# Kernel tuning notes

Measured on AMD Instinct MI355X. Metric: run time of the kernel, lower is better.

## Reference

```python
import jax, jax.numpy as jnp
import numpy as np

B, S, F, H = 4, 8192, 1024, 16
D = F // H  # k_dim = 64
EPS = 1e-6


def setup_inputs() -> dict:
    rng = jax.random.key(0)
    ks = jax.random.split(rng, 6)
    # xavier-normal-ish scale for square (F, F) kernels
    w_std = float(np.sqrt(2.0 / (F + F)))
    return {
        "query": jax.random.normal(ks[0], (B, S, F), jnp.float32),
        "key": jax.random.normal(ks[1], (B, S, F), jnp.float32),
        "value": jax.random.normal(ks[2], (B, S, F), jnp.float32),
        "Wq": jax.random.normal(ks[3], (F, F), jnp.float32) * w_std,
        "Wk": jax.random.normal(ks[4], (F, F), jnp.float32) * w_std,
        "Wv": jax.random.normal(ks[5], (F, F), jnp.float32) * w_std,
        # per-head LayerNorm params for K and V (galerkin branch): (H, D)
        "ln_k_scale": jnp.ones((H, D), jnp.float32),
        "ln_k_bias": jnp.zeros((H, D), jnp.float32),
        "ln_v_scale": jnp.ones((H, D), jnp.float32),
        "ln_v_bias": jnp.zeros((H, D), jnp.float32),
    }


def _per_head_layernorm(x, scale, bias):
    # x: (B, H, N, D); scale/bias: (H, D) -> broadcast per head
    mu = jnp.mean(x, axis=-1, keepdims=True)
    var = jnp.var(x, axis=-1, keepdims=True)
    xn = (x - mu) * jax.lax.rsqrt(var + EPS)
    return xn * scale[None, :, None, :] + bias[None, :, None, :]


def reference(query, key, value, Wq, Wk, Wv, ln_k_scale, ln_k_bias, ln_v_scale, ln_v_bias):
    # QKV projections (no bias), then the module's raw contiguous reshape
    # (B, S, F) -> (B, H, S, D)  [NOT a head transpose -- faithful to source]
    q = jnp.matmul(query, Wq).reshape(B, H, -1, D)
    k = jnp.matmul(key, Wk).reshape(B, H, -1, D)
    v = jnp.matmul(value, Wv).reshape(B, H, -1, D)
    # galerkin: per-head LayerNorm on K and V only
    k = _per_head_layernorm(k, ln_k_scale, ln_k_bias)
    v = _per_head_layernorm(v, ln_v_scale, ln_v_bias)
    # linear (galerkin) attention: p_attn = K^T V / seq_len; out = Q p_attn
    seq_len = v.shape[-2]
    p_attn = jnp.einsum('bhnd,bhne->bhde', k, v) / seq_len  # (B, H, D, D)
    x = jnp.einsum('bhnd,bhde->bhne', q, p_attn)            # (B, H, N, D)
    att_output = x.reshape(B, -1, H * D)                    # (B, S, F)
    return (att_output, p_attn)
```

## Files before the change

### kernel.cpp

```cpp
#include <hip/hip_runtime.h>
#include <hip/hip_bf16.h>
#include <stdint.h>

#define DEVI __device__ __forceinline__

typedef __attribute__((ext_vector_type(8))) short bf16x8;
typedef __attribute__((ext_vector_type(4))) float f32x4;

static constexpr int Bb = 4, Ss = 8192, Ff = 1024, Hh = 16, Dd = 64;
static constexpr int Mm = Bb * Ss;
static constexpr int Kk = Ff;
static constexpr int PROJ_ELEMS = Mm * Ff;

DEVI ushort f2bf(float f) {
  uint32_t u = __builtin_bit_cast(uint32_t, f);
  u += 0x7fffu + ((u >> 16) & 1u);
  return (ushort)(u >> 16);
}
DEVI float bf2f(ushort u) { return __builtin_bit_cast(float, (uint32_t)u << 16); }

DEVI uint32_t pack2(float a, float b) {
  return (uint32_t)f2bf(a) | ((uint32_t)f2bf(b) << 16);
}

DEVI void async16(void* lds, const void* g) {
  __builtin_amdgcn_global_load_lds((const __attribute__((address_space(1))) void*)g,
                                   (__attribute__((address_space(3))) void*)lds,
                                   16, 0, 0);
}

__global__ __launch_bounds__(256) void wt_kernel(const float* __restrict__ Wq,
                                                 const float* __restrict__ Wk,
                                                 const float* __restrict__ Wv,
                                                 ushort* __restrict__ wt) {
  __shared__ float tile[64][65];
  int b = blockIdx.x;
  const int w = b >> 8; b &= 255;
  const int kt = b >> 4, nt = b & 15;
  const float* Wsrc = (w == 0) ? Wq : ((w == 1) ? Wk : Wv);
  ushort* dst = wt + (size_t)w * 1024 * 1024;
  const int t = threadIdx.x;
  const int r = t >> 6, c = t & 63;
#pragma unroll
  for (int i = 0; i < 16; i++) {
    const int kk = kt * 64 + r + i * 4;
    tile[r + i * 4][c] = Wsrc[(size_t)kk * 1024 + nt * 64 + c];
  }
  __syncthreads();
#pragma unroll
  for (int i = 0; i < 16; i++) {
    const int nn = nt * 64 + r + i * 4;
    dst[(size_t)nn * 1024 + kt * 64 + c] = f2bf(tile[c][r + i * 4]);
  }
}

__global__ __launch_bounds__(256, 3) void gemm_qkv_kernel(
    const float* __restrict__ Aq, const float* __restrict__ Ak,
    const float* __restrict__ Av, const ushort* __restrict__ Wt,
    ushort* __restrict__ Cout,
    const float* __restrict__ ksc, const float* __restrict__ kbi,
    const float* __restrict__ vsc, const float* __restrict__ vbi) {
  __shared__ __align__(16) ushort As[128][64];
  __shared__ __align__(16) ushort Bs[128][64];

  const int bx0 = blockIdx.x;
  const int bx = (bx0 & 7) * 768 + (bx0 >> 3);
  const int proj = bx >> 11;
  const int t2 = bx & 2047;
  const int mt = t2 >> 3;
  const int nt = t2 & 7;
  const float* A = (proj == 0) ? Aq : ((proj == 1) ? Ak : Av);
  const ushort* Bw = Wt + (size_t)proj * 1024 * 1024;
  ushort* C = Cout + (size_t)proj * PROJ_ELEMS;
  const int m0 = mt * 128, n0 = nt * 128;
  const int tid = threadIdx.x;
  const int lane = tid & 63;
  const int wave = tid >> 6;
  const int wy = wave >> 1, wx = wave & 1;

  const int ar = tid >> 3;
  const int ac = (tid & 7) * 8;
  const float* Abase = A + (size_t)m0 * Kk;

  const f32x4 fzero = {0.0f, 0.0f, 0.0f, 0.0f};
  f32x4 acc[4][4];
#pragma unroll
  for (int i = 0; i < 4; i++)
#pragma unroll
    for (int j = 0; j < 4; j++) acc[i][j] = fzero;

  for (int k0 = 0; k0 < Kk; k0 += 64) {
#pragma unroll
    for (int j = 0; j < 4; j++) {
      const int seg = wave * 4 + j;
      const int brow = seg * 8 + (lane >> 3);
      const int bcol = (lane & 7) * 8;
      async16(&Bs[seg * 8][0], Bw + (size_t)(n0 + brow) * Kk + k0 + bcol);
    }
#pragma unroll
    for (int i = 0; i < 4; i++) {
      const int row = ar + i * 32;
      const float* src = Abase + (size_t)row * Kk + k0 + ac;
      const float4 f0 = *(const float4*)src;
      const float4 f1 = *(const float4*)(src + 4);
      uint4 v;
      v.x = pack2(f0.x, f0.y);
      v.y = pack2(f0.z, f0.w);
      v.z = pack2(f1.x, f1.y);
      v.w = pack2(f1.z, f1.w);
      *(uint4*)&As[row][ac] = v;
    }
    __syncthreads();
#pragma unroll
    for (int ks = 0; ks < 2; ks++) {
      bf16x8 af[4], bv[4];
#pragma unroll
      for (int i = 0; i < 4; i++)
        af[i] = *(const bf16x8*)&As[wy * 64 + i * 16 + (lane & 15)][ks * 32 + (lane >> 4) * 8];
#pragma unroll
      for (int j = 0; j < 4; j++)
        bv[j] = *(const bf16x8*)&Bs[wx * 64 + j * 16 + (lane & 15)][ks * 32 + (lane >> 4) * 8];
#pragma unroll
      for (int i = 0; i < 4; i++)
#pragma unroll
        for (int j = 0; j < 4; j++)
          acc[i][j] = __builtin_amdgcn_mfma_f32_16x16x32_bf16(af[i], bv[j], acc[i][j], 0, 0, 0);
    }
    __syncthreads();
  }

  if (proj == 0) {
#pragma unroll
    for (int i = 0; i < 4; i++) {
      const int rbase = m0 + wy * 64 + i * 16 + (lane >> 4) * 4;
#pragma unroll
      for (int j = 0; j < 4; j++) {
        const int col = n0 + wx * 64 + j * 16 + (lane & 15);
#pragma unroll
        for (int r = 0; r < 4; r++)
          C[(size_t)(rbase + r) * 1024 + col] = f2bf(acc[i][j][r]);
      }
    }
  } else {
    const float* sc = (proj == 1) ? ksc : vsc;
    const float* bi = (proj == 1) ? kbi : vbi;
    const int h = (m0 >> 9) & 15;
    float scv[4], biv[4];
#pragma unroll
    for (int j = 0; j < 4; j++) {
      const int d = j * 16 + (lane & 15);
      scv[j] = sc[h * 64 + d];
      biv[j] = bi[h * 64 + d];
    }
#pragma unroll
    for (int i = 0; i < 4; i++) {
      const int rbase = m0 + wy * 64 + i * 16 + (lane >> 4) * 4;
#pragma unroll
      for (int r = 0; r < 4; r++) {
        float s = 0.f, sq = 0.f;
#pragma unroll
        for (int j = 0; j < 4; j++) {
          const float x = acc[i][j][r];
          s += x;
          sq += x * x;
        }
        s += __shfl_xor(s, 1); s += __shfl_xor(s, 2);
        s += __shfl_xor(s, 4); s += __shfl_xor(s, 8);
        sq += __shfl_xor(sq, 1); sq += __shfl_xor(sq, 2);
        sq += __shfl_xor(sq, 4); sq += __shfl_xor(sq, 8);
        const float mean = s * (1.0f / 64.0f);
        const float var = sq * (1.0f / 64.0f) - mean * mean;
        const float rs = rsqrtf(var + 1e-6f);
#pragma unroll
        for (int j = 0; j < 4; j++) {
          const int col = n0 + wx * 64 + j * 16 + (lane & 15);
          C[(size_t)(rbase + r) * 1024 + col] =
              f2bf((acc[i][j][r] - mean) * rs * scv[j] + biv[j]);
        }
      }
    }
  }
}

__global__ __launch_bounds__(256) void pattn_kernel(const ushort* __restrict__ kp,
                                                    const ushort* __restrict__ vp,
                                                    float* __restrict__ praw) {
  __shared__ __align__(16) ushort kT[64][72];
  __shared__ __align__(16) ushort vT[64][72];
  const int bh = blockIdx.x >> 5;
  const int nc = blockIdx.x & 31;
  const ushort* kb = kp + ((size_t)bh << 19) + (size_t)nc * 16384;
  const ushort* vb = vp + ((size_t)bh << 19) + (size_t)nc * 16384;
  const int tid = threadIdx.x;
  const int lane = tid & 63;
  const int wave = tid >> 6;
  const int d0 = wave * 16;
  const f32x4 fzero = {0.0f, 0.0f, 0.0f, 0.0f};
  f32x4 acc[4];
#pragma unroll
  for (int e = 0; e < 4; e++) acc[e] = fzero;

  for (int c = 0; c < 4; c++) {
    const ushort* kc = kb + c * 4096;
    const ushort* vc = vb + c * 4096;
    const uint4 ka = *(const uint4*)(kc + (size_t)lane * 64 + d0);
    const uint4 ka2 = *(const uint4*)(kc + (size_t)lane * 64 + d0 + 8);
    const uint4 va = *(const uint4*)(vc + (size_t)lane * 64 + d0);
    const uint4 va2 = *(const uint4*)(vc + (size_t)lane * 64 + d0 + 8);
    __syncthreads();
    const uint32_t* kw = (const uint32_t*)&ka;
    const uint32_t* kw2 = (const uint32_t*)&ka2;
    const uint32_t* vw = (const uint32_t*)&va;
    const uint32_t* vw2 = (const uint32_t*)&va2;
#pragma unroll
    for (int j = 0; j < 4; j++) {
      kT[d0 + 2 * j][lane] = (ushort)(kw[j] & 0xffffu);
      kT[d0 + 2 * j + 1][lane] = (ushort)(kw[j] >> 16);
      kT[d0 + 8 + 2 * j][lane] = (ushort)(kw2[j] & 0xffffu);
      kT[d0 + 8 + 2 * j + 1][lane] = (ushort)(kw2[j] >> 16);
      vT[d0 + 2 * j][lane] = (ushort)(vw[j] & 0xffffu);
      vT[d0 + 2 * j + 1][lane] = (ushort)(vw[j] >> 16);
      vT[d0 + 8 + 2 * j][lane] = (ushort)(vw2[j] & 0xffffu);
      vT[d0 + 8 + 2 * j + 1][lane] = (ushort)(vw2[j] >> 16);
    }
    __syncthreads();
#pragma unroll
    for (int ks = 0; ks < 2; ks++) {
      const bf16x8 af = *(const bf16x8*)&kT[wave * 16 + (lane & 15)][ks * 32 + (lane >> 4) * 8];
#pragma unroll
      for (int e = 0; e < 4; e++) {
        const bf16x8 bv = *(const bf16x8*)&vT[e * 16 + (lane & 15)][ks * 32 + (lane >> 4) * 8];
        acc[e] = __builtin_amdgcn_mfma_f32_16x16x32_bf16(af, bv, acc[e], 0, 0, 0);
      }
    }
  }
#pragma unroll
  for (int e = 0; e < 4; e++)
#pragma unroll
    for (int r = 0; r < 4; r++) {
      const int drow = wave * 16 + (lane >> 4) * 4 + r;
      const int ecol = e * 16 + (lane & 15);
      atomicAdd(&praw[(size_t)bh * 4096 + drow * 64 + ecol], acc[e][r]);
    }
}

__global__ __launch_bounds__(256) void scalep_kernel(const float* __restrict__ praw,
                                                     float* __restrict__ pout) {
  const int i = blockIdx.x * 256 + threadIdx.x;
  pout[i] = praw[i] * (1.0f / 8192.0f);
}

__global__ __launch_bounds__(256) void outgemm_kernel(const ushort* __restrict__ qp,
                                                      const float* __restrict__ praw,
                                                      float* __restrict__ xout) {
  __shared__ __align__(16) ushort pT[64][72];
  const int bh = blockIdx.x >> 4;
  const int mc = blockIdx.x & 15;
  const ushort* qb = qp + ((size_t)bh << 19) + (size_t)mc * 512 * 64;
  float* ob = xout + ((size_t)bh << 19) + (size_t)mc * 512 * 64;
  const float* pb = praw + (size_t)bh * 4096;
  const int tid = threadIdx.x;
  const int lane = tid & 63;
  const int wave = tid >> 6;
  for (int i = tid; i < 4096; i += 256) {
    const int d = i >> 6, e = i & 63;
    pT[e][d] = f2bf(pb[i] * (1.0f / 8192.0f));
  }
  __syncthreads();
  bf16x8 bv[4][2];
#pragma unroll
  for (int e = 0; e < 4; e++)
#pragma unroll
    for (int ks = 0; ks < 2; ks++)
      bv[e][ks] = *(const bf16x8*)&pT[e * 16 + (lane & 15)][ks * 32 + (lane >> 4) * 8];
  const f32x4 fzero = {0.0f, 0.0f, 0.0f, 0.0f};
  for (int it = 0; it < 8; it++) {
    const int rbase = it * 64 + wave * 16;
    const ushort* qrow = qb + (size_t)rbase * 64;
    const bf16x8 a0 = *(const bf16x8*)(qrow + (size_t)(lane & 15) * 64 + (lane >> 4) * 8);
    const bf16x8 a1 = *(const bf16x8*)(qrow + (size_t)(lane & 15) * 64 + (lane >> 4) * 8 + 32);
    f32x4 acc[4];
#pragma unroll
    for (int e = 0; e < 4; e++) acc[e] = fzero;
#pragma unroll
    for (int e = 0; e < 4; e++) {
      acc[e] = __builtin_amdgcn_mfma_f32_16x16x32_bf16(a0, bv[e][0], acc[e], 0, 0, 0);
      acc[e] = __builtin_amdgcn_mfma_f32_16x16x32_bf16(a1, bv[e][1], acc[e], 0, 0, 0);
    }
#pragma unroll
    for (int e = 0; e < 4; e++)
#pragma unroll
      for (int r = 0; r < 4; r++)
        ob[(size_t)(rbase + (lane >> 4) * 4 + r) * 64 + e * 16 + (lane & 15)] = acc[e][r];
  }
}

extern "C" void kernel_launch(void* const* d_in, const int* in_sizes, int n_in,
                              void* d_out, int out_size, void* d_ws, size_t ws_size,
                              hipStream_t stream) {
  const float* q_in = (const float*)d_in[0];
  const float* k_in = (const float*)d_in[1];
  const float* v_in = (const float*)d_in[2];
  const float* Wq = (const float*)d_in[3];
  const float* Wk = (const float*)d_in[4];
  const float* Wv = (const float*)d_in[5];
  const float* ksc = (const float*)d_in[6];
  const float* kbi = (const float*)d_in[7];
  const float* vsc = (const float*)d_in[8];
  const float* vbi = (const float*)d_in[9];

  ushort* q_proj = (ushort*)d_ws;
  ushort* k_proj = q_proj + (size_t)PROJ_ELEMS;
  ushort* v_proj = k_proj + (size_t)PROJ_ELEMS;
  ushort* wtb = v_proj + (size_t)PROJ_ELEMS;
  float* praw = (float*)(wtb + (size_t)3 * 1024 * 1024);

  float* att = (float*)d_out;
  float* pout = att + (size_t)PROJ_ELEMS;

  wt_kernel<<<768, 256, 0, stream>>>(Wq, Wk, Wv, wtb);
  gemm_qkv_kernel<<<6144, 256, 0, stream>>>(q_in, k_in, v_in, wtb, q_proj,
                                            ksc, kbi, vsc, vbi);
  (void)hipMemsetAsync(praw, 0, (size_t)Bb * Hh * 64 * 64 * sizeof(float), stream);
  pattn_kernel<<<2048, 256, 0, stream>>>(k_proj, v_proj, praw);
  scalep_kernel<<<1024, 256, 0, stream>>>(praw, pout);
  outgemm_kernel<<<1024, 256, 0, stream>>>(q_proj, praw, att);
}
```

Baseline: 816.3 us.

## Pre-cast activations to bf16 and stream both GEMM operands asynchronously into LDS

A new kernel converts the fp32 query/key/value activations to bf16 in the workspace. The QKV GEMM can then load both A and B tiles with direct global-to-LDS async copies, and it raises the occupancy hint to 4 blocks per CU. The aim is to remove the in-GEMM fp32 loading and conversion and the repeated fp32 reads across column tiles. The cost is an extra full pass over the activations and a larger workspace, and a fallback legacy path remains for small workspaces. The p_attn and output kernels' grids are also rebalanced: p_attn uses fewer, longer blocks and the output GEMM uses more, shorter ones.

Result: faster. 784.7 us (-3.9%).

```diff
diff --git a/kernel.cpp b/kernel.cpp
--- a/kernel.cpp
+++ b/kernel.cpp
@@ -27,6 +27,29 @@
   __builtin_amdgcn_global_load_lds((const __attribute__((address_space(1))) void*)g,
                                    (__attribute__((address_space(3))) void*)lds,
                                    16, 0, 0);
+}
+
+__global__ __launch_bounds__(256) void cast_kernel(const float* __restrict__ q,
+                                                   const float* __restrict__ k,
+                                                   const float* __restrict__ v,
+                                                   ushort* __restrict__ abf) {
+  const int b = blockIdx.x;
+  const int proj = b >> 11;
+  const float* src = (proj == 0) ? q : ((proj == 1) ? k : v);
+  ushort* dst = abf + (size_t)proj * PROJ_ELEMS;
+  const int tid0 = (b & 2047) * 256 + threadIdx.x;
+#pragma unroll
+  for (int p = 0; p < 8; ++p) {
+    const size_t i = ((size_t)p * 524288 + (size_t)tid0) * 8;
+    const float4 f0 = *(const float4*)(src + i);
+    const float4 f1 = *(const float4*)(src + i + 4);
+    uint4 o;
+    o.x = pack2(f0.x, f0.y);
+    o.y = pack2(f0.z, f0.w);
+    o.z = pack2(f1.x, f1.y);
+    o.w = pack2(f1.z, f1.w);
+    *(uint4*)(dst + i) = o;
+  }
 }
 
 __global__ __launch_bounds__(256) void wt_kernel(const float* __restrict__ Wq,
@@ -54,7 +77,119 @@
   }
 }
 
-__global__ __launch_bounds__(256, 3) void gemm_qkv_kernel(
+__global__ __launch_bounds__(256, 4) void gemm_qkv_kernel(
+    const ushort* __restrict__ Abf, const ushort* __restrict__ Wt,
+    ushort* __restrict__ Cout,
+    const float* __restrict__ ksc, const float* __restrict__ kbi,
+    const float* __restrict__ vsc, const float* __restrict__ vbi) {
+  __shared__ __align__(16) ushort As[128][64];
+  __shared__ __align__(16) ushort Bs[128][64];
+
+  const int bx0 = blockIdx.x;
+  const int bx = (bx0 & 7) * 768 + (bx0 >> 3);
+  const int proj = bx >> 11;
+  const int t2 = bx & 2047;
+  const int mt = t2 >> 3;
+  const int nt = t2 & 7;
+  const ushort* A = Abf + (size_t)proj * PROJ_ELEMS;
+  const ushort* Bw = Wt + (size_t)proj * 1024 * 1024;
+  ushort* C = Cout + (size_t)proj * PROJ_ELEMS;
+  const int m0 = mt * 128, n0 = nt * 128;
+  const int tid = threadIdx.x;
+  const int lane = tid & 63;
+  const int wave = tid >> 6;
+  const int wy = wave >> 1, wx = wave & 1;
+
+  const f32x4 fzero = {0.0f, 0.0f, 0.0f, 0.0f};
+  f32x4 acc[4][4];
+#pragma unroll
+  for (int i = 0; i < 4; i++)
+#pragma unroll
+    for (int j = 0; j < 4; j++) acc[i][j] = fzero;
+
+  const int srow = lane >> 3;
+  const int scol = (lane & 7) * 8;
+
+  for (int k0 = 0; k0 < Kk; k0 += 64) {
+#pragma unroll
+    for (int j = 0; j < 4; j++) {
+      const int seg = wave * 4 + j;
+      async16(&As[seg * 8][0], A + (size_t)(m0 + seg * 8 + srow) * Kk + k0 + scol);
+      async16(&Bs[seg * 8][0], Bw + (size_t)(n0 + seg * 8 + srow) * Kk + k0 + scol);
+    }
+    __syncthreads();
+#pragma unroll
+    for (int ks = 0; ks < 2; ks++) {
+      bf16x8 af[4], bv[4];
+#pragma unroll
+      for (int i = 0; i < 4; i++)
+        af[i] = *(const bf16x8*)&As[wy * 64 + i * 16 + (lane & 15)][ks * 32 + (lane >> 4) * 8];
+#pragma unroll
+      for (int j = 0; j < 4; j++)
+        bv[j] = *(const bf16x8*)&Bs[wx * 64 + j * 16 + (lane & 15)][ks * 32 + (lane >> 4) * 8];
+#pragma unroll
+      for (int i = 0; i < 4; i++)
+#pragma unroll
+        for (int j = 0; j < 4; j++)
+          acc[i][j] = __builtin_amdgcn_mfma_f32_16x16x32_bf16(af[i], bv[j], acc[i][j], 0, 0, 0);
+    }
+    __syncthreads();
+  }
+
+  if (proj == 0) {
+#pragma unroll
+    for (int i = 0; i < 4; i++) {
+      const int rbase = m0 + wy * 64 + i * 16 + (lane >> 4) * 4;
+#pragma unroll
+      for (int j = 0; j < 4; j++) {
+        const int col = n0 + wx * 64 + j * 16 + (lane & 15);
+#pragma unroll
+        for (int r = 0; r < 4; r++)
+          C[(size_t)(rbase + r) * 1024 + col] = f2bf(acc[i][j][r]);
+      }
+    }
+  } else {
+    const float* sc = (proj == 1) ? ksc : vsc;
+    const float* bi = (proj == 1) ? kbi : vbi;
+    const int h = (m0 >> 9) & 15;
+    float scv[4], biv[4];
+#pragma unroll
+    for (int j = 0; j < 4; j++) {
+      const int d = j * 16 + (lane & 15);
+      scv[j] = sc[h * 64 + d];
+      biv[j] = bi[h * 64 + d];
+    }
+#pragma unroll
+    for (int i = 0; i < 4; i++) {
+      const int rbase = m0 + wy * 64 + i * 16 + (lane >> 4) * 4;
+#pragma unroll
+      for (int r = 0; r < 4; r++) {
+        float s = 0.f, sq = 0.f;
+#pragma unroll
+        for (int j = 0; j < 4; j++) {
+          const float x = acc[i][j][r];
+          s += x;
+          sq += x * x;
+        }
+        s += __shfl_xor(s, 1); s += __shfl_xor(s, 2);
+        s += __shfl_xor(s, 4); s += __shfl_xor(s, 8);
+        sq += __shfl_xor(sq, 1); sq += __shfl_xor(sq, 2);
+        sq += __shfl_xor(sq, 4); sq += __shfl_xor(sq, 8);
+        const float mean = s * (1.0f / 64.0f);
+        const float var = sq * (1.0f / 64.0f) - mean * mean;
+        const float rs = rsqrtf(var + 1e-6f);
+#pragma unroll
+        for (int j = 0; j < 4; j++) {
+          const int col = n0 + wx * 64 + j * 16 + (lane & 15);
+          C[(size_t)(rbase + r) * 1024 + col] =
+              f2bf((acc[i][j][r] - mean) * rs * scv[j] + biv[j]);
+        }
+      }
+    }
+  }
+}
+
+__global__ __launch_bounds__(256, 3) void gemm_qkv_legacy(
     const float* __restrict__ Aq, const float* __restrict__ Ak,
     const float* __restrict__ Av, const ushort* __restrict__ Wt,
     ushort* __restrict__ Cout,
@@ -77,7 +212,6 @@
   const int lane = tid & 63;
   const int wave = tid >> 6;
   const int wy = wave >> 1, wx = wave & 1;
-
   const int ar = tid >> 3;
   const int ac = (tid & 7) * 8;
   const float* Abase = A + (size_t)m0 * Kk;
@@ -187,10 +321,10 @@
                                                     float* __restrict__ praw) {
   __shared__ __align__(16) ushort kT[64][72];
   __shared__ __align__(16) ushort vT[64][72];
-  const int bh = blockIdx.x >> 5;
-  const int nc = blockIdx.x & 31;
-  const ushort* kb = kp + ((size_t)bh << 19) + (size_t)nc * 16384;
-  const ushort* vb = vp + ((size_t)bh << 19) + (size_t)nc * 16384;
+  const int bh = blockIdx.x >> 4;
+  const int nc = blockIdx.x & 15;
+  const ushort* kb = kp + ((size_t)bh << 19) + (size_t)nc * 32768;
+  const ushort* vb = vp + ((size_t)bh << 19) + (size_t)nc * 32768;
   const int tid = threadIdx.x;
   const int lane = tid & 63;
   const int wave = tid >> 6;
@@ -200,7 +334,7 @@
 #pragma unroll
   for (int e = 0; e < 4; e++) acc[e] = fzero;
 
-  for (int c = 0; c < 4; c++) {
+  for (int c = 0; c < 8; c++) {
     const ushort* kc = kb + c * 4096;
     const ushort* vc = vb + c * 4096;
     const uint4 ka = *(const uint4*)(kc + (size_t)lane * 64 + d0);
@@ -254,10 +388,10 @@
                                                       const float* __restrict__ praw,
                                                       float* __restrict__ xout) {
   __shared__ __align__(16) ushort pT[64][72];
-  const int bh = blockIdx.x >> 4;
-  const int mc = blockIdx.x & 15;
-  const ushort* qb = qp + ((size_t)bh << 19) + (size_t)mc * 512 * 64;
-  float* ob = xout + ((size_t)bh << 19) + (size_t)mc * 512 * 64;
+  const int bh = blockIdx.x >> 5;
+  const int mc = blockIdx.x & 31;
+  const ushort* qb = qp + ((size_t)bh << 19) + (size_t)mc * 256 * 64;
+  float* ob = xout + ((size_t)bh << 19) + (size_t)mc * 256 * 64;
   const float* pb = praw + (size_t)bh * 4096;
   const int tid = threadIdx.x;
   const int lane = tid & 63;
@@ -274,7 +408,7 @@
     for (int ks = 0; ks < 2; ks++)
       bv[e][ks] = *(const bf16x8*)&pT[e * 16 + (lane & 15)][ks * 32 + (lane >> 4) * 8];
   const f32x4 fzero = {0.0f, 0.0f, 0.0f, 0.0f};
-  for (int it = 0; it < 8; it++) {
+  for (int it = 0; it < 4; it++) {
     const int rbase = it * 64 + wave * 16;
     const ushort* qrow = qb + (size_t)rbase * 64;
     const bf16x8 a0 = *(const bf16x8*)(qrow + (size_t)(lane & 15) * 64 + (lane >> 4) * 8);
@@ -309,20 +443,40 @@
   const float* vsc = (const float*)d_in[8];
   const float* vbi = (const float*)d_in[9];
 
-  ushort* q_proj = (ushort*)d_ws;
-  ushort* k_proj = q_proj + (size_t)PROJ_ELEMS;
-  ushort* v_proj = k_proj + (size_t)PROJ_ELEMS;
-  ushort* wtb = v_proj + (size_t)PROJ_ELEMS;
-  float* praw = (float*)(wtb + (size_t)3 * 1024 * 1024);
-
   float* att = (float*)d_out;
   float* pout = att + (size_t)PROJ_ELEMS;
 
-  wt_kernel<<<768, 256, 0, stream>>>(Wq, Wk, Wv, wtb);
-  gemm_qkv_kernel<<<6144, 256, 0, stream>>>(q_in, k_in, v_in, wtb, q_proj,
-                                            ksc, kbi, vsc, vbi);
-  (void)hipMemsetAsync(praw, 0, (size_t)Bb * Hh * 64 * 64 * sizeof(float), stream);
-  pattn_kernel<<<2048, 256, 0, stream>>>(k_proj, v_proj, praw);
-  scalep_kernel<<<1024, 256, 0, stream>>>(praw, pout);
-  outgemm_kernel<<<1024, 256, 0, stream>>>(q_proj, praw, att);
-}
+  const size_t need_new = (size_t)3 * PROJ_ELEMS * 2 * 2
+                        + (size_t)3 * 1024 * 1024 * 2
+                        + (size_t)262144 * 4;
+  if (ws_size >= need_new) {
+    ushort* a_bf = (ushort*)d_ws;
+    ushort* q_proj = a_bf + (size_t)3 * PROJ_ELEMS;
+    ushort* k_proj = q_proj + (size_t)PROJ_ELEMS;
+    ushort* v_proj = k_proj + (size_t)PROJ_ELEMS;
+    ushort* wtb = v_proj + (size_t)PROJ_ELEMS;
+    float* praw = (float*)(wtb + (size_t)3 * 1024 * 1024);
+
+    wt_kernel<<<768, 256, 0, stream>>>(Wq, Wk, Wv, wtb);
+    cast_kernel<<<6144, 256, 0, stream>>>(q_in, k_in, v_in, a_bf);
+    gemm_qkv_kernel<<<6144, 256, 0, stream>>>(a_bf, wtb, q_proj, ksc, kbi, vsc, vbi);
+    (void)hipMemsetAsync(praw, 0, (size_t)Bb * Hh * 64 * 64 * sizeof(float), stream);
+    pattn_kernel<<<1024, 256, 0, stream>>>(k_proj, v_proj, praw);
+    scalep_kernel<<<1024, 256, 0, stream>>>(praw, pout);
+    outgemm_kernel<<<2048, 256, 0, stream>>>(q_proj, praw, att);
+  } else {
+    ushort* q_proj = (ushort*)d_ws;
+    ushort* k_proj = q_proj + (size_t)PROJ_ELEMS;
+    ushort* v_proj = k_proj + (size_t)PROJ_ELEMS;
+    ushort* wtb = v_proj + (size_t)PROJ_ELEMS;
+    float* praw = (float*)(wtb + (size_t)3 * 1024 * 1024);
+
+    wt_kernel<<<768, 256, 0, stream>>>(Wq, Wk, Wv, wtb);
+    gemm_qkv_legacy<<<6144, 256, 0, stream>>>(q_in, k_in, v_in, wtb, q_proj,
+                                              ksc, kbi, vsc, vbi);
+    (void)hipMemsetAsync(praw, 0, (size_t)Bb * Hh * 64 * 64 * sizeof(float), stream);
+    pattn_kernel<<<1024, 256, 0, stream>>>(k_proj, v_proj, praw);
+    scalep_kernel<<<1024, 256, 0, stream>>>(praw, pout);
+    outgemm_kernel<<<2048, 256, 0, stream>>>(q_proj, praw, att);
+  }
+}
```
